# Optimization experiments

Hardware: AMD Instinct MI355X
Metric: run time of the kernel (lower is better)

Reference implementation:

```python
import jax, jax.numpy as jnp
import numpy as np

L = 524288      # input_length (~33 s @ 16 kHz)
C = 129         # cochlear channels
DS = 80         # downsample rate = sr / (1000 / frame_length)


def setup_inputs() -> dict:
    key = jax.random.key(0)
    k0, k1, k2 = jax.random.split(key, 3)
    x = jax.random.normal(k0, (L,), dtype=jnp.float32)
    # Filterbank transfer functions (stand-in for cochlear_filter_params.npz)
    Hs_real = 0.1 * jax.random.normal(k1, (C, L), dtype=jnp.float32)
    Hs_imag = 0.1 * jax.random.normal(k2, (C, L), dtype=jnp.float32)
    alpha_comp = jnp.full((C,), 0.9, dtype=jnp.float32)
    alpha_leak = jnp.array(0.9922179, dtype=jnp.float32)
    li_kernel = jnp.array([1.0, -1.0], dtype=jnp.float32)  # first-difference conv kernel
    return {"x": x, "Hs_real": Hs_real, "Hs_imag": Hs_imag,
            "alpha_comp": alpha_comp, "alpha_leak": alpha_leak,
            "li_kernel": li_kernel}


def reference(x, Hs_real, Hs_imag, alpha_comp, alpha_leak, li_kernel):
    # 1. Cochlear filterbank: FFT -> per-channel complex multiply -> IFFT
    X = jnp.fft.fft(x)                                   # [L] complex
    Hs = Hs_real + 1j * Hs_imag                          # [C, L]
    coch = jnp.fft.ifft(Hs * X[None, :], axis=-1).real   # [C, L]

    # 2. Power-law compression per channel: |x|^a * sign(x)
    comp = jnp.abs(coch) ** alpha_comp[:, None] * jnp.sign(coch)

    # 3-4. LIN: first difference along channel axis (SAME pad -> zero row at end), then ReLU
    shifted = jnp.concatenate([comp[1:], jnp.zeros_like(comp[:1])], axis=0)
    lin = jax.nn.relu(comp * li_kernel[0] + shifted * li_kernel[1])

    # 5. Leaky integration via FFT-domain filtering, then downsample
    freqs = jnp.fft.fftfreq(L).astype(jnp.float32) * (2.0 * jnp.pi)
    Hleak = 1.0 / (1.0 - alpha_leak * (jnp.cos(freqs) - 1j * jnp.sin(freqs)))  # [L]
    out = jnp.fft.ifft(Hleak[None, :] * jnp.fft.fft(lin, axis=-1), axis=-1).real
    return out[:, DS - 1::DS]                            # [C, L // DS]
```

## Files before the change

### kernel.cpp

```cpp
#include <hip/hip_runtime.h>
#include <math.h>

#define LN    524288
#define N1    512
#define N2    1024
#define NCH   129
#define DSR   80
#define NOUT  6553
#define OB2   64
#define NBLK  103
#define SPB   (OB2*DSR)
#define TPW   20
#define NPAIR 65
#define KTAIL 48
#define SB    1024
#define LMAP(i) ((i) + ((i) >> 3))
#define SWZ(p)  ((p) ^ ((((p) >> 5) & 1) * 31))

__device__ __forceinline__ float2 cmulf(float2 a, float2 b) {
    return make_float2(a.x*b.x - a.y*b.y, a.x*b.y + a.y*b.x);
}

__device__ __forceinline__ float powsign(float x, float a) {
    float m = __builtin_amdgcn_exp2f(a * __builtin_amdgcn_logf(fabsf(x)));
    return copysignf(m, x);
}

__global__ void pack_x(const float* __restrict__ x, float2* __restrict__ dst) {
    int i = blockIdx.x * 256 + threadIdx.x;
    dst[i] = make_float2(x[i], 0.f);
}

__global__ void transpose_c(const float2* __restrict__ src, float2* __restrict__ dst,
                            int R, int Cc) {
    __shared__ float2 tile[32][33];
    size_t boff = (size_t)blockIdx.z * LN;
    src += boff; dst += boff;
    int x  = blockIdx.x * 32 + threadIdx.x;
    int y0 = blockIdx.y * 32 + threadIdx.y;
#pragma unroll
    for (int i = 0; i < 32; i += 8)
        tile[threadIdx.y + i][threadIdx.x] = src[(size_t)(y0 + i) * Cc + x];
    __syncthreads();
    int xo  = blockIdx.y * 32 + threadIdx.x;
    int yo0 = blockIdx.x * 32 + threadIdx.y;
#pragma unroll
    for (int i = 0; i < 32; i += 8)
        dst[(size_t)(yo0 + i) * R + xo] = tile[threadIdx.x][threadIdx.y + i];
}

template<int M, int SIGN, int TW>
__global__ __launch_bounds__(256) void fft_rows(const float2* __restrict__ src,
                                                float2* __restrict__ dst,
                                                int rows_per_batch) {
    __shared__ __align__(16) float2 ping[M];
    __shared__ __align__(16) float2 pong[M];
    __shared__ float2 twid[M];
    size_t rowg = blockIdx.x;
    const float2* srow = src + rowg * M;
    float2* drow = dst + rowg * M;
    int row = (int)(rowg % (size_t)rows_per_batch);
    int t = threadIdx.x;
    const float4* s4 = (const float4*)srow;
    for (int ii = t; ii < M/2; ii += 256)
        *(float4*)&ping[2*ii] = s4[ii];
    for (int i = t; i < M; i += 256) {
        if (i >= 1) {
            int h = 1 << (31 - __clz((unsigned)i));
            float ang = (float)SIGN * 3.14159265358979323846f * (float)(i - h) / (float)h;
            float s, c; __sincosf(ang, &s, &c);
            twid[i] = make_float2(c, s);
        }
    }
    __syncthreads();
    float2* a = ping;
    float2* b = pong;
    for (int Ns = 1; Ns < M; Ns <<= 1) {
        for (int j = t; j < M/2; j += 256) {
            int jm = j & (Ns - 1);
            float2 v0 = a[j];
            float2 v1 = a[j + M/2];
            float2 tw = twid[Ns + jm];
            float2 w = make_float2(v1.x*tw.x - v1.y*tw.y, v1.x*tw.y + v1.y*tw.x);
            int d0 = ((j & ~(Ns - 1)) << 1) | jm;
            b[d0]      = make_float2(v0.x + w.x, v0.y + w.y);
            b[d0 + Ns] = make_float2(v0.x - w.x, v0.y - w.y);
        }
        __syncthreads();
        float2* tmp = a; a = b; b = tmp;
    }
    if (TW) {
        const float c2pi = 6.28318530717958647692f / (float)LN;
        for (int i = t; i < M; i += 256) {
            float2 v = a[i];
            unsigned prod = ((unsigned)row * (unsigned)i) & (unsigned)(LN - 1);
            float ang = (float)SIGN * c2pi * (float)prod;
            float s, c;
            __sincosf(ang, &s, &c);
            drow[i] = make_float2(v.x*c - v.y*s, v.x*s + v.y*c);
        }
    } else {
        float4* d4 = (float4*)drow;
        for (int ii = t; ii < M/2; ii += 256)
            d4[ii] = *(const float4*)&a[2*ii];
    }
}

__device__ __forceinline__ void herm2(float2 X1,
                                      float har,  float hai,  float hbr,  float hbi,
                                      float har2, float hai2, float hbr2, float hbi2,
                                      bool hasB, float2& Wk, float2& WkL) {
    float2 a1 = make_float2(har*X1.x - hai*X1.y, har*X1.y + hai*X1.x);
    float2 a2 = make_float2(har2*X1.x + hai2*X1.y, hai2*X1.x - har2*X1.y);
    float yar = 0.5f*(a1.x + a2.x), yai = 0.5f*(a1.y - a2.y);
    float ybr = 0.f, ybi = 0.f;
    if (hasB) {
        float2 b1 = make_float2(hbr*X1.x - hbi*X1.y, hbr*X1.y + hbi*X1.x);
        float2 b2 = make_float2(hbr2*X1.x + hbi2*X1.y, hbi2*X1.x - hbr2*X1.y);
        ybr = 0.5f*(b1.x + b2.x); ybi = 0.5f*(b1.y - b2.y);
    }
    Wk  = make_float2(yar - ybi, yai + ybr);
    WkL = make_float2(yar + ybi, ybr - yai);
}

__global__ __launch_bounds__(256) void build_w4(const float* __restrict__ Hr,
                                                const float* __restrict__ Hi,
                                                const float2* __restrict__ X,
                                                float2* __restrict__ W, int pair0) {
    __shared__ float lowS[4][1160];
    __shared__ float mirS[4][1160];
    int s0 = blockIdx.x * SB;
    int pl = blockIdx.y;
    int p  = pair0 + pl;
    int ca = 2*p, cb = 2*p + 1;
    bool hasB = (cb < NCH);
    const float* Hs0 = Hr + (size_t)ca * LN;
    const float* Hs1 = Hi + (size_t)ca * LN;
    const float* Hs2 = hasB ? (Hr + (size_t)cb * LN) : Hs0;
    const float* Hs3 = hasB ? (Hi + (size_t)cb * LN) : Hs1;
    const float* Hs[4] = {Hs0, Hs1, Hs2, Hs3};
    float2* Wp = W + (size_t)pl * LN;
    int t = threadIdx.x;
    int j4 = 4 * t;
    int mbase = LN - s0 - SB;

#pragma unroll
    for (int a = 0; a < 4; a++) {
        float4 lv = *(const float4*)&Hs[a][s0 + j4];
        float4 mv = *(const float4*)&Hs[a][mbase + j4];
        int lm = LMAP(j4);
        lowS[a][lm+0] = lv.x; lowS[a][lm+1] = lv.y; lowS[a][lm+2] = lv.z; lowS[a][lm+3] = lv.w;
        mirS[a][lm+0] = mv.x; mirS[a][lm+1] = mv.y; mirS[a][lm+2] = mv.z; mirS[a][lm+3] = mv.w;
    }
    if (t == 0) {
#pragma unroll
        for (int a = 0; a < 4; a++) lowS[a][LMAP(SB)] = Hs[a][s0 + SB];
    }
    if (t == 1 && s0 > 0) {
#pragma unroll
        for (int a = 0; a < 4; a++) mirS[a][LMAP(SB)] = Hs[a][LN - s0];
    }
    __syncthreads();

    float4 xa = *(const float4*)&X[s0 + j4];
    float4 xb = *(const float4*)&X[s0 + j4 + 2];
    float2 wlo[4];
#pragma unroll
    for (int d = 0; d < 4; d++) {
        int k = s0 + j4 + d;
        float2 Xk = (d == 0) ? make_float2(xa.x, xa.y) :
                    (d == 1) ? make_float2(xa.z, xa.w) :
                    (d == 2) ? make_float2(xb.x, xb.y) : make_float2(xb.z, xb.w);
        if (k == 0) {
            float2 Ya = cmulf(make_float2(lowS[0][0], lowS[1][0]), Xk);
            float br = 0.f;
            if (hasB) { float2 Yb = cmulf(make_float2(lowS[2][0], lowS[3][0]), Xk); br = Yb.x; }
            wlo[d] = make_float2(Ya.x, br);
        } else {
            int jl = LMAP(j4 + d);
            int jm = LMAP(SB - j4 - d);
            float2 Wk, WkL;
            herm2(Xk, lowS[0][jl], lowS[1][jl], lowS[2][jl], lowS[3][jl],
                      mirS[0][jm], mirS[1][jm], mirS[2][jm], mirS[3][jm], hasB, Wk, WkL);
            wlo[d] = Wk;
        }
    }
    *(float4*)&Wp[s0 + j4]     = make_float4(wlo[0].x, wlo[0].y, wlo[1].x, wlo[1].y);
    *(float4*)&Wp[s0 + j4 + 2] = make_float4(wlo[2].x, wlo[2].y, wlo[3].x, wlo[3].y);

    float2 wmi[4];
#pragma unroll
    for (int d = 0; d < 4; d++) {
        int m = mbase + j4 + d;
        if (m == LN/2) {
            float2 Xv = X[LN/2];
            float2 Ya = cmulf(make_float2(mirS[0][0], mirS[1][0]), Xv);
            float br = 0.f;
            if (hasB) { float2 Yb = cmulf(make_float2(mirS[2][0], mirS[3][0]), Xv); br = Yb.x; }
            wmi[d] = make_float2(Ya.x, br);
        } else {
            int kp = LN - m;
            int jl = LMAP(SB - j4 - d);
            int jm = LMAP(j4 + d);
            float2 Xk = X[kp];
            float2 Wk, WkL;
            herm2(Xk, lowS[0][jl], lowS[1][jl], lowS[2][jl], lowS[3][jl],
                      mirS[0][jm], mirS[1][jm], mirS[2][jm], mirS[3][jm], hasB, Wk, WkL);
            wmi[d] = WkL;
        }
    }
    *(float4*)&Wp[mbase + j4]     = make_float4(wmi[0].x, wmi[0].y, wmi[1].x, wmi[1].y);
    *(float4*)&Wp[mbase + j4 + 2] = make_float4(wmi[2].x, wmi[2].y, wmi[3].x, wmi[3].y);
}

__global__ __launch_bounds__(1024) void kB(float2* __restrict__ D1) {
    __shared__ float sRe[16][545];
    __shared__ float sIm[16][545];
    __shared__ float2 twid[512];
    int cg = blockIdx.x;
    int pl = blockIdx.y;
    float2* Dp = D1 + (size_t)pl * LN;
    unsigned c_base = 16u * cg;
    int t = threadIdx.x;

    if (t >= 1 && t < 512) {
        int h = 1 << (31 - __clz((unsigned)t));
        float ang = 3.14159265358979323846f * (float)(t - h) / (float)h;
        float s, c; __sincosf(ang, &s, &c);
        twid[t] = make_float2(c, s);
    }

    int cc = t & 15;
    int g  = (t >> 4) & 3;
    int w  = t >> 6;

#pragma unroll
    for (int i = 0; i < 8; i++) {
        int r = w + (g << 4) + (i << 6);
        float2 v = Dp[(size_t)r * N2 + c_base + cc];
        int sp = SWZ(r);
        sRe[cc][sp] = v.x;
        sIm[cc][sp] = v.y;
    }
    __syncthreads();

    int cc2 = t >> 6;
    int l   = t & 63;
    for (int h = 256; h >= 1; h >>= 1) {
#pragma unroll
        for (int i = 0; i < 4; i++) {
            int j = l + (i << 6);
            int q = j & (h - 1);
            int base = ((j & ~(h - 1)) << 1) | q;
            float2 tw = twid[h + q];
            int p0 = SWZ(base), p1 = SWZ(base + h);
            float are = sRe[cc2][p0], aim = sIm[cc2][p0];
            float bre = sRe[cc2][p1], bim = sIm[cc2][p1];
            sRe[cc2][p0] = are + bre;  sIm[cc2][p0] = aim + bim;
            float dre = are - bre, dim = aim - bim;
            sRe[cc2][p1] = dre*tw.x - dim*tw.y;
            sIm[cc2][p1] = dre*tw.y + dim*tw.x;
        }
        __syncthreads();
    }

    const float c2pi = 6.28318530717958647692f / (float)LN;
    unsigned truec = c_base + (unsigned)cc;
#pragma unroll
    for (int i = 0; i < 8; i++) {
        int pos = w + (g << 4) + (i << 6);
        unsigned jj = __brev((unsigned)pos) >> 23;
        int sp = SWZ(pos);
        float re = sRe[cc][sp], im = sIm[cc][sp];
        unsigned prod = (jj * truec) & (unsigned)(LN - 1);
        float ang = c2pi * (float)prod;
        float s, c;
        __sincosf(ang, &s, &c);
        Dp[(size_t)jj * N2 + truec] = make_float2(re*c - im*s, re*s + im*c);
    }
}

__global__ __launch_bounds__(256) void ifft_finish(const float2* __restrict__ src,
                                                   float* __restrict__ comp,
                                                   const float* __restrict__ alpha_comp,
                                                   int pair0) {
    __shared__ __align__(16) float2 tile[32][33];
    int pl = blockIdx.z;
    int p = pair0 + pl;
    int ca = 2*p, cb = 2*p + 1;
    const float2* s = src + (size_t)pl * LN;
    int m0 = blockIdx.x * 32, j0 = blockIdx.y * 32;
    int tx = threadIdx.x, ty = threadIdx.y;
    int tid = ty * 8 + tx;
    int jl = tid >> 3, mq = tid & 7;
    const float4* row4 = (const float4*)&s[(size_t)(j0 + jl) * N2 + m0 + mq * 4];
    float4 a = row4[0], b = row4[1];
    tile[jl][mq*4+0] = make_float2(a.x, a.y);
    tile[jl][mq*4+1] = make_float2(a.z, a.w);
    tile[jl][mq*4+2] = make_float2(b.x, b.y);
    tile[jl][mq*4+3] = make_float2(b.z, b.w);
    __syncthreads();
    float aa = alpha_comp[ca];
    float ab = (cb < NCH) ? alpha_comp[cb] : 1.f;
    const float invL = 1.f / (float)LN;
    float oa[4], ob[4];
#pragma unroll
    for (int d = 0; d < 4; d++) {
        float2 v = tile[4*tx + d][ty];
        oa[d] = powsign(v.x * invL, aa);
        ob[d] = powsign(v.y * invL, ab);
    }
    size_t n0 = (size_t)(m0 + ty) * N1 + j0 + 4*tx;
    *(float4*)&comp[(size_t)ca * LN + n0] = make_float4(oa[0], oa[1], oa[2], oa[3]);
    if (cb < NCH)
        *(float4*)&comp[(size_t)cb * LN + n0] = make_float4(ob[0], ob[1], ob[2], ob[3]);
}

__global__ __launch_bounds__(256) void iir_part1(
    const float* __restrict__ comp, const float* __restrict__ alpha_leak,
    const float* __restrict__ li_kernel, float* __restrict__ out,
    float* __restrict__ carryOut) {
    __shared__ float win[SPB + SPB/TPW];
    __shared__ float wv[4], wg[4];
    int blk = blockIdx.x;
    int c = blockIdx.y;
    int t = threadIdx.x;
    float alpha = alpha_leak[0];
    float k0 = li_kernel[0], k1 = li_kernel[1];
    int base = blk * SPB;
    const int cap = NOUT * DSR;
    const float* c0 = comp + (size_t)c * LN;
    const float* c1 = (c + 1 < NCH) ? comp + (size_t)(c + 1) * LN : nullptr;
    const float4 z4 = make_float4(0.f, 0.f, 0.f, 0.f);
    for (int i4 = 4*t; i4 < SPB; i4 += 1024) {
        int g = base + i4;
        float4 u0 = *(const float4*)&c0[g];
        float4 u1 = c1 ? *(const float4*)&c1[g] : z4;
        float vv[4] = {k0*u0.x + k1*u1.x, k0*u0.y + k1*u1.y,
                       k0*u0.z + k1*u1.z, k0*u0.w + k1*u1.w};
#pragma unroll
        for (int d = 0; d < 4; d++) {
            float v = fmaxf(vv[d], 0.f);
            if (g + d >= cap) v = 0.f;
            int i = i4 + d;
            win[i + i / TPW] = v;
        }
    }
    __syncthreads();
    float v = 0.f;
    int lbase = 21 * t;
#pragma unroll
    for (int i = 0; i < TPW; i++)
        v = fmaf(alpha, v, win[lbase + i]);
    float g = powf(alpha, (float)TPW);
    int lid = t & 63, wid = t >> 6;
#pragma unroll
    for (int d = 1; d < 64; d <<= 1) {
        float pv = __shfl_up(v, d);
        float pg = __shfl_up(g, d);
        if (lid >= d) { v = fmaf(g, pv, v); g = g * pg; }
    }
    if (lid == 63) { wv[wid] = v; wg[wid] = g; }
    __syncthreads();
    float cv = 0.f;
#pragma unroll
    for (int w = 0; w < 3; w++)
        if (w < wid) cv = wv[w] + wg[w] * cv;
    float vf = fmaf(g, cv, v);
    int nact = NOUT - blk * OB2; if (nact > OB2) nact = OB2;
    if ((t & 3) == 3) {
        int o = t >> 2;
        if (o < nact)
            out[(size_t)c * NOUT + blk * OB2 + o] = vf;
    }
    if (t == 4 * nact - 1)
        carryOut[c * NBLK + blk] = vf;
}

__global__ void iir_part2(const float* __restrict__ comp, const float* __restrict__ alpha_leak,
                          const float* __restrict__ li_kernel,
                          const float* __restrict__ carryOut, float* __restrict__ D) {
    int c = threadIdx.x;
    if (c >= NCH) return;
    float alpha = alpha_leak[0];
    float k0 = li_kernel[0], k1 = li_kernel[1];
    const float* c0 = comp + (size_t)c * LN;
    const float* c1 = (c + 1 < NCH) ? comp + (size_t)(c + 1) * LN : nullptr;
    float tail = 0.f, ap = 1.f;
    for (int j = 0; j < KTAIL; j++) {
        int g = LN - 1 - j;
        float u0 = c0[g];
        float u1 = c1 ? c1[g] : 0.f;
        float v = k0 * u0 + k1 * u1; v = v > 0.f ? v : 0.f;
        tail += ap * v;
        ap *= alpha;
    }
    float D0 = tail + ap * carryOut[c * NBLK + (NBLK - 1)]
             + powf(alpha, (float)(KTAIL + 2000)) * carryOut[c * NBLK + (NBLK - 2)];
    D[c * NBLK + 0] = D0;
    for (int b = 1; b < NBLK; b++)
        D[c * NBLK + b] = carryOut[c * NBLK + b - 1];
}

__global__ void iir_part3(const float* __restrict__ D, const float* __restrict__ alpha_leak,
                          float* __restrict__ out) {
    int idx = blockIdx.x * 256 + threadIdx.x;
    if (idx >= NCH * NOUT) return;
    int c = idx / NOUT, m = idx - c * NOUT;
    int b = m / OB2, o = m - b * OB2;
    float alpha = alpha_leak[0];
    float beta = powf(alpha, (float)DSR);
    float dec = powf(beta, (float)(o + 1));
    out[idx] += dec * D[c * NBLK + b];
}

extern "C" void kernel_launch(void* const* d_in, const int* in_sizes, int n_in,
                              void* d_out, int out_size, void* d_ws, size_t ws_size,
                              hipStream_t stream) {
    const float* x  = (const float*)d_in[0];
    const float* Hr = (const float*)d_in[1];
    const float* Hi = (const float*)d_in[2];
    const float* ac = (const float*)d_in[3];
    const float* al = (const float*)d_in[4];
    const float* li = (const float*)d_in[5];
    float* out = (float*)d_out;

    char* ws = (char*)d_ws;
    size_t off = 0;
    auto alloc = [&](size_t bytes) -> void* {
        void* p = ws + off;
        off += (bytes + 255) & ~(size_t)255;
        return p;
    };
    float2* Xf     = (float2*)alloc((size_t)LN * sizeof(float2));
    float*  comp   = (float*) alloc((size_t)NCH * LN * sizeof(float));
    float*  cOut   = (float*) alloc((size_t)NCH * NBLK * sizeof(float));
    float*  Dbuf   = (float*) alloc((size_t)NCH * NBLK * sizeof(float));
    size_t remain = (ws_size > off) ? (ws_size - off) : 0;
    int chunk = (int)(remain / ((size_t)LN * sizeof(float2)));
    if (chunk > NPAIR) chunk = NPAIR;
    if (chunk < 2)     chunk = 2;
    float2* bufA = (float2*)alloc((size_t)chunk * LN * sizeof(float2));

    dim3 tb(32, 8, 1);

    float2* fA = bufA;
    float2* fB = bufA + LN;
    pack_x<<<LN / 256, 256, 0, stream>>>(x, fA);
    transpose_c<<<dim3(N2/32, N1/32, 1), tb, 0, stream>>>(fA, fB, N1, N2);
    fft_rows<N1, -1, 1><<<N2, 256, 0, stream>>>(fB, fB, N2);
    transpose_c<<<dim3(N1/32, N2/32, 1), tb, 0, stream>>>(fB, fA, N2, N1);
    fft_rows<N2, -1, 0><<<N1, 256, 0, stream>>>(fA, fA, N1);
    transpose_c<<<dim3(N2/32, N1/32, 1), tb, 0, stream>>>(fA, Xf, N1, N2);

    for (int ci = 0; ci < NPAIR; ci += chunk) {
        int np = NPAIR - ci; if (np > chunk) np = chunk;
        build_w4<<<dim3(LN/2/SB, np), 256, 0, stream>>>(Hr, Hi, Xf, bufA, ci);
        kB<<<dim3(64, np), 1024, 0, stream>>>(bufA);
        fft_rows<N2, 1, 0><<<N1 * np, 256, 0, stream>>>(bufA, bufA, N1);
        ifft_finish<<<dim3(32, 16, np), dim3(8, 32), 0, stream>>>(bufA, comp, ac, ci);
    }

    iir_part1<<<dim3(NBLK, NCH, 1), 256, 0, stream>>>(comp, al, li, out, cOut);
    iir_part2<<<1, 256, 0, stream>>>(comp, al, li, cOut, Dbuf);
    iir_part3<<<(NCH * NOUT + 255) / 256, 256, 0, stream>>>(Dbuf, al, out);
}
```

Baseline: 665.4 us.

## Fuse spectrum build into first column FFT pass of inverse transform

Removes the separate build_w4 kernel and computes the packed two-channel Hermitian spectrum directly inside the column-FFT kernel, which now reads H, X and their mirrored entries straight from global memory. This drops one full write and read of the intermediate complex buffer per channel pair. It also pairs mirrored column groups on adjacent blocks so that mirror reads hit nearby data. The trade-off is strided, column-wise gathers of H (4 bytes per element at a 4 KB stride) in place of coalesced float4 loads, which could hurt memory efficiency.

```diff
diff --git a/kernel.cpp b/kernel.cpp
--- a/kernel.cpp
+++ b/kernel.cpp
@@ -13,8 +13,6 @@
 #define TPW   20
 #define NPAIR 65
 #define KTAIL 48
-#define SB    1024
-#define LMAP(i) ((i) + ((i) >> 3))
 #define SWZ(p)  ((p) ^ ((((p) >> 5) & 1) * 31))
 
 __device__ __forceinline__ float2 cmulf(float2 a, float2 b) {
@@ -123,104 +121,26 @@
     WkL = make_float2(yar + ybi, ybr - yai);
 }
 
-__global__ __launch_bounds__(256) void build_w4(const float* __restrict__ Hr,
-                                                const float* __restrict__ Hi,
-                                                const float2* __restrict__ X,
-                                                float2* __restrict__ W, int pair0) {
-    __shared__ float lowS[4][1160];
-    __shared__ float mirS[4][1160];
-    int s0 = blockIdx.x * SB;
+__global__ __launch_bounds__(1024) void kBW2(const float* __restrict__ Hr,
+                                             const float* __restrict__ Hi,
+                                             const float2* __restrict__ X,
+                                             float2* __restrict__ D1, int pair0) {
+    __shared__ float sRe[16][545];
+    __shared__ float sIm[16][545];
+    __shared__ float2 twid[512];
+    int bx = blockIdx.x;
+    int qq = bx >> 1;
+    int bb = (bx & 1) ? (63 - qq) : qq;
     int pl = blockIdx.y;
     int p  = pair0 + pl;
     int ca = 2*p, cb = 2*p + 1;
     bool hasB = (cb < NCH);
-    const float* Hs0 = Hr + (size_t)ca * LN;
-    const float* Hs1 = Hi + (size_t)ca * LN;
-    const float* Hs2 = hasB ? (Hr + (size_t)cb * LN) : Hs0;
-    const float* Hs3 = hasB ? (Hi + (size_t)cb * LN) : Hs1;
-    const float* Hs[4] = {Hs0, Hs1, Hs2, Hs3};
-    float2* Wp = W + (size_t)pl * LN;
-    int t = threadIdx.x;
-    int j4 = 4 * t;
-    int mbase = LN - s0 - SB;
-
-#pragma unroll
-    for (int a = 0; a < 4; a++) {
-        float4 lv = *(const float4*)&Hs[a][s0 + j4];
-        float4 mv = *(const float4*)&Hs[a][mbase + j4];
-        int lm = LMAP(j4);
-        lowS[a][lm+0] = lv.x; lowS[a][lm+1] = lv.y; lowS[a][lm+2] = lv.z; lowS[a][lm+3] = lv.w;
-        mirS[a][lm+0] = mv.x; mirS[a][lm+1] = mv.y; mirS[a][lm+2] = mv.z; mirS[a][lm+3] = mv.w;
-    }
-    if (t == 0) {
-#pragma unroll
-        for (int a = 0; a < 4; a++) lowS[a][LMAP(SB)] = Hs[a][s0 + SB];
-    }
-    if (t == 1 && s0 > 0) {
-#pragma unroll
-        for (int a = 0; a < 4; a++) mirS[a][LMAP(SB)] = Hs[a][LN - s0];
-    }
-    __syncthreads();
-
-    float4 xa = *(const float4*)&X[s0 + j4];
-    float4 xb = *(const float4*)&X[s0 + j4 + 2];
-    float2 wlo[4];
-#pragma unroll
-    for (int d = 0; d < 4; d++) {
-        int k = s0 + j4 + d;
-        float2 Xk = (d == 0) ? make_float2(xa.x, xa.y) :
-                    (d == 1) ? make_float2(xa.z, xa.w) :
-                    (d == 2) ? make_float2(xb.x, xb.y) : make_float2(xb.z, xb.w);
-        if (k == 0) {
-            float2 Ya = cmulf(make_float2(lowS[0][0], lowS[1][0]), Xk);
-            float br = 0.f;
-            if (hasB) { float2 Yb = cmulf(make_float2(lowS[2][0], lowS[3][0]), Xk); br = Yb.x; }
-            wlo[d] = make_float2(Ya.x, br);
-        } else {
-            int jl = LMAP(j4 + d);
-            int jm = LMAP(SB - j4 - d);
-            float2 Wk, WkL;
-            herm2(Xk, lowS[0][jl], lowS[1][jl], lowS[2][jl], lowS[3][jl],
-                      mirS[0][jm], mirS[1][jm], mirS[2][jm], mirS[3][jm], hasB, Wk, WkL);
-            wlo[d] = Wk;
-        }
-    }
-    *(float4*)&Wp[s0 + j4]     = make_float4(wlo[0].x, wlo[0].y, wlo[1].x, wlo[1].y);
-    *(float4*)&Wp[s0 + j4 + 2] = make_float4(wlo[2].x, wlo[2].y, wlo[3].x, wlo[3].y);
-
-    float2 wmi[4];
-#pragma unroll
-    for (int d = 0; d < 4; d++) {
-        int m = mbase + j4 + d;
-        if (m == LN/2) {
-            float2 Xv = X[LN/2];
-            float2 Ya = cmulf(make_float2(mirS[0][0], mirS[1][0]), Xv);
-            float br = 0.f;
-            if (hasB) { float2 Yb = cmulf(make_float2(mirS[2][0], mirS[3][0]), Xv); br = Yb.x; }
-            wmi[d] = make_float2(Ya.x, br);
-        } else {
-            int kp = LN - m;
-            int jl = LMAP(SB - j4 - d);
-            int jm = LMAP(j4 + d);
-            float2 Xk = X[kp];
-            float2 Wk, WkL;
-            herm2(Xk, lowS[0][jl], lowS[1][jl], lowS[2][jl], lowS[3][jl],
-                      mirS[0][jm], mirS[1][jm], mirS[2][jm], mirS[3][jm], hasB, Wk, WkL);
-            wmi[d] = WkL;
-        }
-    }
-    *(float4*)&Wp[mbase + j4]     = make_float4(wmi[0].x, wmi[0].y, wmi[1].x, wmi[1].y);
-    *(float4*)&Wp[mbase + j4 + 2] = make_float4(wmi[2].x, wmi[2].y, wmi[3].x, wmi[3].y);
-}
-
-__global__ __launch_bounds__(1024) void kB(float2* __restrict__ D1) {
-    __shared__ float sRe[16][545];
-    __shared__ float sIm[16][545];
-    __shared__ float2 twid[512];
-    int cg = blockIdx.x;
-    int pl = blockIdx.y;
+    const float* HaR = Hr + (size_t)ca * LN;
+    const float* HaI = Hi + (size_t)ca * LN;
+    const float* HbR = hasB ? (Hr + (size_t)cb * LN) : HaR;
+    const float* HbI = hasB ? (Hi + (size_t)cb * LN) : HaI;
     float2* Dp = D1 + (size_t)pl * LN;
-    unsigned c_base = 16u * cg;
+    unsigned c_base = 16u * bb;
     int t = threadIdx.x;
 
     if (t >= 1 && t < 512) {
@@ -233,14 +153,33 @@
     int cc = t & 15;
     int g  = (t >> 4) & 3;
     int w  = t >> 6;
+    int c  = (int)c_base + cc;
+    bool isC0 = (c == 0);
+    int cm = isC0 ? 0 : (1024 - c);
 
 #pragma unroll
     for (int i = 0; i < 8; i++) {
-        int r = w + (g << 4) + (i << 6);
-        float2 v = Dp[(size_t)r * N2 + c_base + cc];
+        int r  = w + (g << 4) + (i << 6);
+        int rm = isC0 ? ((512 - r) & 511) : (511 - r);
+        int k  = (r  << 10) + c;
+        int kL = (rm << 10) + cm;
+        float2 Xk = X[k];
+        float har = HaR[k],  hai = HaI[k],  hbr = HbR[k],  hbi = HbI[k];
+        float har2 = HaR[kL], hai2 = HaI[kL], hbr2 = HbR[kL], hbi2 = HbI[kL];
+        float re, im;
+        if (k == 0 || k == LN/2) {
+            float2 Ya = cmulf(make_float2(har, hai), Xk);
+            float br = 0.f;
+            if (hasB) { float2 Yb = cmulf(make_float2(hbr, hbi), Xk); br = Yb.x; }
+            re = Ya.x; im = br;
+        } else {
+            float2 Wk, WkL;
+            herm2(Xk, har, hai, hbr, hbi, har2, hai2, hbr2, hbi2, hasB, Wk, WkL);
+            re = Wk.x; im = Wk.y;
+        }
         int sp = SWZ(r);
-        sRe[cc][sp] = v.x;
-        sIm[cc][sp] = v.y;
+        sRe[cc][sp] = re;
+        sIm[cc][sp] = im;
     }
     __syncthreads();
 
@@ -274,9 +213,9 @@
         float re = sRe[cc][sp], im = sIm[cc][sp];
         unsigned prod = (jj * truec) & (unsigned)(LN - 1);
         float ang = c2pi * (float)prod;
-        float s, c;
-        __sincosf(ang, &s, &c);
-        Dp[(size_t)jj * N2 + truec] = make_float2(re*c - im*s, re*s + im*c);
+        float s, c2;
+        __sincosf(ang, &s, &c2);
+        Dp[(size_t)jj * N2 + truec] = make_float2(re*c2 - im*s, re*s + im*c2);
     }
 }
 
@@ -455,8 +394,7 @@
 
     for (int ci = 0; ci < NPAIR; ci += chunk) {
         int np = NPAIR - ci; if (np > chunk) np = chunk;
-        build_w4<<<dim3(LN/2/SB, np), 256, 0, stream>>>(Hr, Hi, Xf, bufA, ci);
-        kB<<<dim3(64, np), 1024, 0, stream>>>(bufA);
+        kBW2<<<dim3(64, np), 1024, 0, stream>>>(Hr, Hi, Xf, bufA, ci);
         fft_rows<N2, 1, 0><<<N1 * np, 256, 0, stream>>>(bufA, bufA, N1);
         ifft_finish<<<dim3(32, 16, np), dim3(8, 32), 0, stream>>>(bufA, comp, ac, ci);
     }
```

After: 851.1 us. +27.9%, slower.
